# Kernel tuning notes

Measured on AMD Instinct MI355X. Metric: run time of the kernel, lower is better.

The kernel has to match this reference:

```python
import jax, jax.numpy as jnp
import numpy as np
from jax import lax

EPS = 1e-8
TAU = 1.0  # step=0 < tau_warmup_steps -> tau = tau_init


def setup_inputs() -> dict:
    key = jax.random.key(0)
    k1, k2 = jax.random.split(key)
    B, D, H, W = 4, 256, 32, 32
    C, K, d = 8, 1024, 32  # n_codebooks, vocab_size, codebook_dim (D = C*d)
    z = jax.random.normal(k1, (B, D, H, W), dtype=jnp.float32)
    cb = jax.random.normal(k2, (C, K, d), dtype=jnp.float32)
    cb = cb / (jnp.linalg.norm(cb, axis=-1, keepdims=True) + 1e-12) * np.sqrt(d).astype(np.float32)
    return {"z": z, "codebooks": cb}


def reference(z, codebooks):
    # Training-mode forward of LGQuantizer (step=0).
    B, D, H, W = z.shape
    C, K, d = codebooks.shape
    # (b d h w) -> (b h w) (c d_sub): chunk along channel dim
    zf = z.transpose(0, 2, 3, 1).reshape(-1, C, d)  # [N, C, d]
    N = zf.shape[0]

    # pairwise squared distances per codebook: [N, C, K]
    z_sq = jnp.sum(zf * zf, axis=-1)                      # [N, C]
    cb_sq = jnp.sum(codebooks * codebooks, axis=-1)       # [C, K]
    cross = jnp.einsum('ncd,ckd->nck', zf, codebooks)     # [N, C, K]
    dists = z_sq[:, :, None] - 2.0 * cross + cb_sq[None, :, :]

    inv_temp = 1.0 / (2.0 * TAU * TAU + EPS)
    logits = -dists * inv_temp
    q = jax.nn.softmax(logits, axis=-1)                   # [N, C, K]

    # soft quantization + straight-through with hard lookup
    z_q = jnp.einsum('nck,ckd->ncd', q, codebooks)        # [N, C, d]
    idx = jnp.argmin(dists, axis=-1)                      # [N, C]
    z_q_hard = codebooks[jnp.arange(C)[None, :], idx]     # [N, C, d]
    z_q_st = z_q + lax.stop_gradient(z_q_hard - z_q)

    quantized = z_q_st.reshape(B, H, W, D).transpose(0, 3, 1, 2)  # [B, D, H, W]
    indices = idx.reshape(B, H, W, C).transpose(0, 3, 1, 2)       # [B, C, H, W]

    # commitment: mse(z_part, q.detach() @ cb.detach()), averaged over codebooks
    commitment = jnp.mean((zf - lax.stop_gradient(z_q)) ** 2)

    log_q = jnp.log(q + EPS)
    neg_ent = jnp.sum(q * log_q, axis=-1)                 # [N, C]
    expected_dist = jnp.mean(jnp.sum(q * dists, axis=-1), axis=0)  # [C]
    kl_uniform = jnp.mean(neg_ent, axis=0) + np.log(K).astype(np.float32)  # [C]
    free_energy = jnp.mean(expected_dist * inv_temp + kl_uniform)

    confidence_loss = jnp.mean(-neg_ent)

    q_bar = jnp.mean(q, axis=0)                           # [C, K]
    balance_loss = jnp.mean(jnp.sum(q_bar * jnp.log(q_bar * K + EPS), axis=-1))

    return (quantized, indices, q, commitment, free_energy,
            confidence_loss, balance_loss, jnp.float32(TAU))
```

## Files before the change

kernel.cpp:

```cpp
#include <hip/hip_runtime.h>

#define WS_A0 0
#define WS_A1 1
#define WS_A2 2
#define WS_QBAR 16
#define WS_CBSQ (WS_QBAR + 8192)
#define WS_IDX  (WS_CBSQ + 8192)

#define OUT_IDX  1048576
#define OUT_Q    1081344
#define OUT_SCAL 34635776

__global__ __launch_bounds__(256) void k_cbsq(const float* __restrict__ cb,
                                              float* __restrict__ ws_f) {
  int i = blockIdx.x * 256 + threadIdx.x;
  const float* r = cb + (size_t)i * 32;
  float s = 0.f;
#pragma unroll
  for (int d = 0; d < 32; ++d) s = fmaf(r[d], r[d], s);
  ws_f[WS_CBSQ + i] = s;
}

__device__ __forceinline__ float wsum64(float v) {
#pragma unroll
  for (int m = 32; m >= 1; m >>= 1) v += __shfl_xor(v, m, 64);
  return v;
}

__device__ __forceinline__ float uread(float v) {
  return __int_as_float(__builtin_amdgcn_readfirstlane(__float_as_int(v)));
}

#define ZLD 33
__global__ __launch_bounds__(1024, 4)
void k_main(
    const float* __restrict__ z, const float* __restrict__ cb,
    float* __restrict__ out, float* __restrict__ ws_f, int* __restrict__ ws_i) {
  __shared__ __attribute__((aligned(16))) float smem[39040];
  float* cb_lds   = smem;
  float* qsum     = smem + 32768;
  float* cbsq_lds = smem + 33792;
  float* z_lds    = smem + 34816;

  const int c    = blockIdx.x >> 5;
  const int nblk = blockIdx.x & 31;
  const int tid  = threadIdx.x;
  const int lane = tid & 63;
  const int wave = tid >> 6;

  const int bb   = (nblk * 128) >> 10;
  const int hwb  = (nblk * 128) & 1023;

  const float4* cb4 = (const float4*)(cb + (size_t)c * 32768);
  float4* lds4 = (float4*)cb_lds;
#pragma unroll
  for (int i = 0; i < 8; ++i) {
    int idx = i * 1024 + tid;
    int k = idx >> 3, q = idx & 7;
    lds4[(k << 3) + (q ^ (k & 7))] = cb4[idx];
  }
  qsum[tid] = 0.f;
  cbsq_lds[tid] = ws_f[WS_CBSQ + c * 1024 + tid];
  {
    const float* zbase = z + (((size_t)bb * 256 + c * 32) << 10) + hwb;
#pragma unroll
    for (int i = 0; i < 4; ++i) {
      int idx = i * 1024 + tid;
      int d = idx >> 7, j = idx & 127;
      z_lds[j * ZLD + d] = zbase[(size_t)d * 1024 + j];
    }
  }
  __syncthreads();

  float* out_q   = out + OUT_Q;
  float* out_idx = out + OUT_IDX;

  float accA0 = 0.f, accA1 = 0.f, accA2 = 0.f;
  const int kl7 = lane & 7;

#pragma unroll 1
  for (int pp = 0; pp < 4; ++pp) {
    const int nl0 = wave * 8 + pp * 2;
    const int nl1 = nl0 + 1;
    const int n0 = nblk * 128 + nl0;
    const int n1 = n0 + 1;

    float zv0[32], zv1[32];
#pragma unroll
    for (int d = 0; d < 32; ++d) {
      zv0[d] = uread(z_lds[nl0 * ZLD + d]);
      zv1[d] = uread(z_lds[nl1 * ZLD + d]);
    }
    float zs0 = 0.f, zs1 = 0.f;
#pragma unroll
    for (int d = 0; d < 32; ++d) {
      zs0 = fmaf(zv0[d], zv0[d], zs0);
      zs1 = fmaf(zv1[d], zv1[d], zs1);
    }

    float e0[16], e1[16];
    float S0 = 0.f, S1 = 0.f, es0 = 0.f, es1 = 0.f;
    float sm0 = -INFINITY, sm1 = -INFINITY;
    int km0 = 0, km1 = 0;

#pragma unroll 2
    for (int jj = 0; jj < 16; ++jj) {
      const int k = jj * 64 + lane;
      float cq = cbsq_lds[k];
      float a0 = 0.f, a1 = 0.f;
      float g0 = 0.f, g1 = 0.f;
#pragma unroll
      for (int q = 0; q < 8; ++q) {
        float4 r4 = lds4[(k << 3) + (q ^ kl7)];
        a0 = fmaf(r4.x, zv0[q * 4 + 0], a0);
        a1 = fmaf(r4.y, zv0[q * 4 + 1], a1);
        a0 = fmaf(r4.z, zv0[q * 4 + 2], a0);
        a1 = fmaf(r4.w, zv0[q * 4 + 3], a1);
        g0 = fmaf(r4.x, zv1[q * 4 + 0], g0);
        g1 = fmaf(r4.y, zv1[q * 4 + 1], g1);
        g0 = fmaf(r4.z, zv1[q * 4 + 2], g0);
        g1 = fmaf(r4.w, zv1[q * 4 + 3], g1);
      }
      float s0 = (a0 + a1) - 0.5f * cq;
      float s1 = (g0 + g1) - 0.5f * cq;
      float ev0 = __expf(s0), ev1 = __expf(s1);
      e0[jj] = ev0; e1[jj] = ev1;
      S0 += ev0;  S1 += ev1;
      es0 = fmaf(ev0, s0, es0);
      es1 = fmaf(ev1, s1, es1);
      if (s0 > sm0) { sm0 = s0; km0 = k; }
      if (s1 > sm1) { sm1 = s1; km1 = k; }
    }

    float St0 = wsum64(S0), St1 = wsum64(S1);
    float rS0 = 1.f / St0, rS1 = 1.f / St1;
    float est0 = wsum64(es0), est1 = wsum64(es1);

    accA1 += (zs0 - 2.f * est0 * rS0) + (zs1 - 2.f * est1 * rS1);
    accA2 += (est0 * rS0 - __logf(St0)) + (est1 * rS1 - __logf(St1));

#pragma unroll
    for (int m = 32; m >= 1; m >>= 1) {
      float so = __shfl_xor(sm0, m, 64); int ko = __shfl_xor(km0, m, 64);
      if (so > sm0 || (so == sm0 && ko < km0)) { sm0 = so; km0 = ko; }
      float sp = __shfl_xor(sm1, m, 64); int kp = __shfl_xor(km1, m, 64);
      if (sp > sm1 || (sp == sm1 && kp < km1)) { sm1 = sp; km1 = kp; }
    }
    if (lane == 0) {
      out_idx[(size_t)bb * 8192 + c * 1024 + hwb + nl0] = (float)km0;
      ws_i[WS_IDX + n0 * 8 + c] = km0;
      out_idx[(size_t)bb * 8192 + c * 1024 + hwb + nl1] = (float)km1;
      ws_i[WS_IDX + n1 * 8 + c] = km1;
    }

    float* qp0 = out_q + ((size_t)n0 * 8 + c) * 1024;
    float* qp1 = out_q + ((size_t)n1 * 8 + c) * 1024;
#pragma unroll 2
    for (int jj = 0; jj < 16; ++jj) {
      float qv0 = e0[jj] * rS0;
      float qv1 = e1[jj] * rS1;
      qp0[jj * 64 + lane] = qv0;
      qp1[jj * 64 + lane] = qv1;
      atomicAdd(&qsum[jj * 64 + lane], qv0 + qv1);
    }

    float dA0, dA1;
    {
      float zqA0[16], zqA1[16];
#pragma unroll
      for (int i = 0; i < 16; ++i) { zqA0[i] = 0.f; zqA1[i] = 0.f; }
#pragma unroll 2
      for (int jj = 0; jj < 16; ++jj) {
        const int k = jj * 64 + lane;
        float qv0 = qp0[jj * 64 + lane];
        float qv1 = qp1[jj * 64 + lane];
#pragma unroll
        for (int q = 0; q < 4; ++q) {
          float4 r4 = lds4[(k << 3) + (q ^ kl7)];
          zqA0[q * 4 + 0] = fmaf(qv0, r4.x, zqA0[q * 4 + 0]);
          zqA0[q * 4 + 1] = fmaf(qv0, r4.y, zqA0[q * 4 + 1]);
          zqA0[q * 4 + 2] = fmaf(qv0, r4.z, zqA0[q * 4 + 2]);
          zqA0[q * 4 + 3] = fmaf(qv0, r4.w, zqA0[q * 4 + 3]);
          zqA1[q * 4 + 0] = fmaf(qv1, r4.x, zqA1[q * 4 + 0]);
          zqA1[q * 4 + 1] = fmaf(qv1, r4.y, zqA1[q * 4 + 1]);
          zqA1[q * 4 + 2] = fmaf(qv1, r4.z, zqA1[q * 4 + 2]);
          zqA1[q * 4 + 3] = fmaf(qv1, r4.w, zqA1[q * 4 + 3]);
        }
      }
#pragma unroll
      for (int t = 0; t < 4; ++t) {
        const int half = 8 >> t;
        const int up = (lane >> (5 - t)) & 1;
#pragma unroll
        for (int i = 0; i < half; ++i) {
          float sa0 = up ? zqA0[i] : zqA0[i + half];
          float ka0 = up ? zqA0[i + half] : zqA0[i];
          zqA0[i] = ka0 + __shfl_xor(sa0, 32 >> t, 64);
          float sa1 = up ? zqA1[i] : zqA1[i + half];
          float ka1 = up ? zqA1[i + half] : zqA1[i];
          zqA1[i] = ka1 + __shfl_xor(sa1, 32 >> t, 64);
        }
      }
      zqA0[0] += __shfl_xor(zqA0[0], 2, 64);
      zqA0[0] += __shfl_xor(zqA0[0], 1, 64);
      zqA1[0] += __shfl_xor(zqA1[0], 2, 64);
      zqA1[0] += __shfl_xor(zqA1[0], 1, 64);
      const int ddA = (lane >> 2) & 15;
      dA0 = z_lds[nl0 * ZLD + ddA] - zqA0[0];
      dA1 = z_lds[nl1 * ZLD + ddA] - zqA1[0];
    }

    float dB0, dB1;
    {
      float zqB0[16], zqB1[16];
#pragma unroll
      for (int i = 0; i < 16; ++i) { zqB0[i] = 0.f; zqB1[i] = 0.f; }
#pragma unroll 2
      for (int jj = 0; jj < 16; ++jj) {
        const int k = jj * 64 + lane;
        float qv0 = qp0[jj * 64 + lane];
        float qv1 = qp1[jj * 64 + lane];
#pragma unroll
        for (int q = 4; q < 8; ++q) {
          float4 r4 = lds4[(k << 3) + (q ^ kl7)];
          const int i0 = (q - 4) * 4;
          zqB0[i0 + 0] = fmaf(qv0, r4.x, zqB0[i0 + 0]);
          zqB0[i0 + 1] = fmaf(qv0, r4.y, zqB0[i0 + 1]);
          zqB0[i0 + 2] = fmaf(qv0, r4.z, zqB0[i0 + 2]);
          zqB0[i0 + 3] = fmaf(qv0, r4.w, zqB0[i0 + 3]);
          zqB1[i0 + 0] = fmaf(qv1, r4.x, zqB1[i0 + 0]);
          zqB1[i0 + 1] = fmaf(qv1, r4.y, zqB1[i0 + 1]);
          zqB1[i0 + 2] = fmaf(qv1, r4.z, zqB1[i0 + 2]);
          zqB1[i0 + 3] = fmaf(qv1, r4.w, zqB1[i0 + 3]);
        }
      }
#pragma unroll
      for (int t = 0; t < 4; ++t) {
        const int half = 8 >> t;
        const int up = (lane >> (5 - t)) & 1;
#pragma unroll
        for (int i = 0; i < half; ++i) {
          float sa0 = up ? zqB0[i] : zqB0[i + half];
          float ka0 = up ? zqB0[i + half] : zqB0[i];
          zqB0[i] = ka0 + __shfl_xor(sa0, 32 >> t, 64);
          float sa1 = up ? zqB1[i] : zqB1[i + half];
          float ka1 = up ? zqB1[i + half] : zqB1[i];
          zqB1[i] = ka1 + __shfl_xor(sa1, 32 >> t, 64);
        }
      }
      zqB0[0] += __shfl_xor(zqB0[0], 2, 64);
      zqB0[0] += __shfl_xor(zqB0[0], 1, 64);
      zqB1[0] += __shfl_xor(zqB1[0], 2, 64);
      zqB1[0] += __shfl_xor(zqB1[0], 1, 64);
      const int ddB = (lane >> 2) & 15;
      dB0 = z_lds[nl0 * ZLD + 16 + ddB] - zqB0[0];
      dB1 = z_lds[nl1 * ZLD + 16 + ddB] - zqB1[0];
    }

    accA0 += 0.25f * wsum64(dA0 * dA0 + dA1 * dA1 + dB0 * dB0 + dB1 * dB1);
  }

  if (lane == 0) {
    atomicAdd(&ws_f[WS_A0], accA0);
    atomicAdd(&ws_f[WS_A1], accA1);
    atomicAdd(&ws_f[WS_A2], accA2);
  }

  __syncthreads();
  atomicAdd(&ws_f[WS_QBAR + c * 1024 + tid], qsum[tid]);
}

__global__ __launch_bounds__(256) void k_hard(const float* __restrict__ cb,
                                              const int* __restrict__ ws_i,
                                              float* __restrict__ out0) {
  int o = blockIdx.x * 256 + threadIdx.x;
  int b  = o >> 18;
  int r  = o & 262143;
  int ch = r >> 10;
  int hw = r & 1023;
  int c = ch >> 5, dd = ch & 31;
  int n = (b << 10) + hw;
  int k = ws_i[WS_IDX + n * 8 + c];
  out0[o] = cb[((size_t)(c << 10) + k) * 32 + dd];
}

__global__ __launch_bounds__(256) void k_final(const float* __restrict__ ws_f,
                                               float* __restrict__ out_s) {
  __shared__ float red[256];
  int tid = threadIdx.x;
  float bal = 0.f;
  for (int i = tid; i < 8192; i += 256) {
    float qb = ws_f[WS_QBAR + i] * (1.0f / 4096.0f);
    bal += qb * __logf(qb * 1024.0f + 1e-8f);
  }
  red[tid] = bal;
  __syncthreads();
  for (int s = 128; s > 0; s >>= 1) {
    if (tid < s) red[tid] += red[tid + s];
    __syncthreads();
  }
  if (tid == 0) {
    float A0 = ws_f[WS_A0], A1 = ws_f[WS_A1], A2 = ws_f[WS_A2];
    out_s[0] = A0 * (1.0f / 1048576.0f);
    out_s[1] = (0.5f * A1 + A2) * (1.0f / 32768.0f) + 6.93147180559945f;
    out_s[2] = -A2 * (1.0f / 32768.0f);
    out_s[3] = red[0] * 0.125f;
    out_s[4] = 1.0f;
  }
}

extern "C" void kernel_launch(void* const* d_in, const int* in_sizes, int n_in,
                              void* d_out, int out_size, void* d_ws, size_t ws_size,
                              hipStream_t stream) {
  (void)in_sizes; (void)n_in; (void)out_size; (void)ws_size;
  const float* z  = (const float*)d_in[0];
  const float* cb = (const float*)d_in[1];
  float* out  = (float*)d_out;
  float* ws_f = (float*)d_ws;
  int*   ws_i = (int*)d_ws;

  hipMemsetAsync(d_ws, 0, (WS_QBAR + 8192) * sizeof(float), stream);
  k_cbsq <<<32,   256, 0, stream>>>(cb, ws_f);
  k_main <<<256, 1024, 0, stream>>>(z, cb, out, ws_f, ws_i);
  k_hard <<<4096, 256, 0, stream>>>(cb, ws_i, out);
  k_final<<<1,    256, 0, stream>>>(ws_f, out + OUT_SCAL);
}
```

Measured before the change: 504.7 us.

## Fuse soft-quantization accumulation into distance passes, recompute logits instead of storing exps

The per-row loop becomes two passes over the codebook. The first pass computes the logits and exp sums and also accumulates the first half of the unnormalized z_q, scaled by 1/S afterwards. The second pass recomputes the logits, writes normalized q with nontemporal stores, tracks the argmax, and accumulates the second half of z_q. This drops the 16-entry exp register arrays and the re-read of q from global memory, at the cost of computing the distance dot products twice. Register pressure should fall and occupancy may rise, but extra FMAs and LDS reads are added.

```diff
diff --git a/kernel.cpp b/kernel.cpp
--- a/kernel.cpp
+++ b/kernel.cpp
@@ -98,20 +98,19 @@
       zs1 = fmaf(zv1[d], zv1[d], zs1);
     }
 
-    float e0[16], e1[16];
     float S0 = 0.f, S1 = 0.f, es0 = 0.f, es1 = 0.f;
-    float sm0 = -INFINITY, sm1 = -INFINITY;
-    int km0 = 0, km1 = 0;
-
-#pragma unroll 2
+    float zqA0[16], zqA1[16];
+#pragma unroll
+    for (int i = 0; i < 16; ++i) { zqA0[i] = 0.f; zqA1[i] = 0.f; }
+
+#pragma unroll 1
     for (int jj = 0; jj < 16; ++jj) {
       const int k = jj * 64 + lane;
-      float cq = cbsq_lds[k];
-      float a0 = 0.f, a1 = 0.f;
-      float g0 = 0.f, g1 = 0.f;
+      const int kbase = k << 3;
+      float a0 = 0.f, a1 = 0.f, g0 = 0.f, g1 = 0.f;
 #pragma unroll
       for (int q = 0; q < 8; ++q) {
-        float4 r4 = lds4[(k << 3) + (q ^ kl7)];
+        float4 r4 = lds4[kbase + (q ^ kl7)];
         a0 = fmaf(r4.x, zv0[q * 4 + 0], a0);
         a1 = fmaf(r4.y, zv0[q * 4 + 1], a1);
         a0 = fmaf(r4.z, zv0[q * 4 + 2], a0);
@@ -121,15 +120,25 @@
         g0 = fmaf(r4.z, zv1[q * 4 + 2], g0);
         g1 = fmaf(r4.w, zv1[q * 4 + 3], g1);
       }
+      float cq = cbsq_lds[k];
       float s0 = (a0 + a1) - 0.5f * cq;
       float s1 = (g0 + g1) - 0.5f * cq;
       float ev0 = __expf(s0), ev1 = __expf(s1);
-      e0[jj] = ev0; e1[jj] = ev1;
       S0 += ev0;  S1 += ev1;
       es0 = fmaf(ev0, s0, es0);
       es1 = fmaf(ev1, s1, es1);
-      if (s0 > sm0) { sm0 = s0; km0 = k; }
-      if (s1 > sm1) { sm1 = s1; km1 = k; }
+#pragma unroll
+      for (int q = 0; q < 4; ++q) {
+        float4 r4 = lds4[kbase + (q ^ kl7)];
+        zqA0[q * 4 + 0] = fmaf(ev0, r4.x, zqA0[q * 4 + 0]);
+        zqA0[q * 4 + 1] = fmaf(ev0, r4.y, zqA0[q * 4 + 1]);
+        zqA0[q * 4 + 2] = fmaf(ev0, r4.z, zqA0[q * 4 + 2]);
+        zqA0[q * 4 + 3] = fmaf(ev0, r4.w, zqA0[q * 4 + 3]);
+        zqA1[q * 4 + 0] = fmaf(ev1, r4.x, zqA1[q * 4 + 0]);
+        zqA1[q * 4 + 1] = fmaf(ev1, r4.y, zqA1[q * 4 + 1]);
+        zqA1[q * 4 + 2] = fmaf(ev1, r4.z, zqA1[q * 4 + 2]);
+        zqA1[q * 4 + 3] = fmaf(ev1, r4.w, zqA1[q * 4 + 3]);
+      }
     }
 
     float St0 = wsum64(S0), St1 = wsum64(S1);
@@ -139,54 +148,7 @@
     accA1 += (zs0 - 2.f * est0 * rS0) + (zs1 - 2.f * est1 * rS1);
     accA2 += (est0 * rS0 - __logf(St0)) + (est1 * rS1 - __logf(St1));
 
-#pragma unroll
-    for (int m = 32; m >= 1; m >>= 1) {
-      float so = __shfl_xor(sm0, m, 64); int ko = __shfl_xor(km0, m, 64);
-      if (so > sm0 || (so == sm0 && ko < km0)) { sm0 = so; km0 = ko; }
-      float sp = __shfl_xor(sm1, m, 64); int kp = __shfl_xor(km1, m, 64);
-      if (sp > sm1 || (sp == sm1 && kp < km1)) { sm1 = sp; km1 = kp; }
-    }
-    if (lane == 0) {
-      out_idx[(size_t)bb * 8192 + c * 1024 + hwb + nl0] = (float)km0;
-      ws_i[WS_IDX + n0 * 8 + c] = km0;
-      out_idx[(size_t)bb * 8192 + c * 1024 + hwb + nl1] = (float)km1;
-      ws_i[WS_IDX + n1 * 8 + c] = km1;
-    }
-
-    float* qp0 = out_q + ((size_t)n0 * 8 + c) * 1024;
-    float* qp1 = out_q + ((size_t)n1 * 8 + c) * 1024;
-#pragma unroll 2
-    for (int jj = 0; jj < 16; ++jj) {
-      float qv0 = e0[jj] * rS0;
-      float qv1 = e1[jj] * rS1;
-      qp0[jj * 64 + lane] = qv0;
-      qp1[jj * 64 + lane] = qv1;
-      atomicAdd(&qsum[jj * 64 + lane], qv0 + qv1);
-    }
-
-    float dA0, dA1;
     {
-      float zqA0[16], zqA1[16];
-#pragma unroll
-      for (int i = 0; i < 16; ++i) { zqA0[i] = 0.f; zqA1[i] = 0.f; }
-#pragma unroll 2
-      for (int jj = 0; jj < 16; ++jj) {
-        const int k = jj * 64 + lane;
-        float qv0 = qp0[jj * 64 + lane];
-        float qv1 = qp1[jj * 64 + lane];
-#pragma unroll
-        for (int q = 0; q < 4; ++q) {
-          float4 r4 = lds4[(k << 3) + (q ^ kl7)];
-          zqA0[q * 4 + 0] = fmaf(qv0, r4.x, zqA0[q * 4 + 0]);
-          zqA0[q * 4 + 1] = fmaf(qv0, r4.y, zqA0[q * 4 + 1]);
-          zqA0[q * 4 + 2] = fmaf(qv0, r4.z, zqA0[q * 4 + 2]);
-          zqA0[q * 4 + 3] = fmaf(qv0, r4.w, zqA0[q * 4 + 3]);
-          zqA1[q * 4 + 0] = fmaf(qv1, r4.x, zqA1[q * 4 + 0]);
-          zqA1[q * 4 + 1] = fmaf(qv1, r4.y, zqA1[q * 4 + 1]);
-          zqA1[q * 4 + 2] = fmaf(qv1, r4.z, zqA1[q * 4 + 2]);
-          zqA1[q * 4 + 3] = fmaf(qv1, r4.w, zqA1[q * 4 + 3]);
-        }
-      }
 #pragma unroll
       for (int t = 0; t < 4; ++t) {
         const int half = 8 >> t;
@@ -206,58 +168,97 @@
       zqA1[0] += __shfl_xor(zqA1[0], 2, 64);
       zqA1[0] += __shfl_xor(zqA1[0], 1, 64);
       const int ddA = (lane >> 2) & 15;
-      dA0 = z_lds[nl0 * ZLD + ddA] - zqA0[0];
-      dA1 = z_lds[nl1 * ZLD + ddA] - zqA1[0];
-    }
-
-    float dB0, dB1;
-    {
-      float zqB0[16], zqB1[16];
-#pragma unroll
-      for (int i = 0; i < 16; ++i) { zqB0[i] = 0.f; zqB1[i] = 0.f; }
-#pragma unroll 2
-      for (int jj = 0; jj < 16; ++jj) {
-        const int k = jj * 64 + lane;
-        float qv0 = qp0[jj * 64 + lane];
-        float qv1 = qp1[jj * 64 + lane];
-#pragma unroll
-        for (int q = 4; q < 8; ++q) {
-          float4 r4 = lds4[(k << 3) + (q ^ kl7)];
-          const int i0 = (q - 4) * 4;
-          zqB0[i0 + 0] = fmaf(qv0, r4.x, zqB0[i0 + 0]);
-          zqB0[i0 + 1] = fmaf(qv0, r4.y, zqB0[i0 + 1]);
-          zqB0[i0 + 2] = fmaf(qv0, r4.z, zqB0[i0 + 2]);
-          zqB0[i0 + 3] = fmaf(qv0, r4.w, zqB0[i0 + 3]);
-          zqB1[i0 + 0] = fmaf(qv1, r4.x, zqB1[i0 + 0]);
-          zqB1[i0 + 1] = fmaf(qv1, r4.y, zqB1[i0 + 1]);
-          zqB1[i0 + 2] = fmaf(qv1, r4.z, zqB1[i0 + 2]);
-          zqB1[i0 + 3] = fmaf(qv1, r4.w, zqB1[i0 + 3]);
-        }
-      }
-#pragma unroll
-      for (int t = 0; t < 4; ++t) {
-        const int half = 8 >> t;
-        const int up = (lane >> (5 - t)) & 1;
-#pragma unroll
-        for (int i = 0; i < half; ++i) {
-          float sa0 = up ? zqB0[i] : zqB0[i + half];
-          float ka0 = up ? zqB0[i + half] : zqB0[i];
-          zqB0[i] = ka0 + __shfl_xor(sa0, 32 >> t, 64);
-          float sa1 = up ? zqB1[i] : zqB1[i + half];
-          float ka1 = up ? zqB1[i + half] : zqB1[i];
-          zqB1[i] = ka1 + __shfl_xor(sa1, 32 >> t, 64);
-        }
-      }
-      zqB0[0] += __shfl_xor(zqB0[0], 2, 64);
-      zqB0[0] += __shfl_xor(zqB0[0], 1, 64);
-      zqB1[0] += __shfl_xor(zqB1[0], 2, 64);
-      zqB1[0] += __shfl_xor(zqB1[0], 1, 64);
-      const int ddB = (lane >> 2) & 15;
-      dB0 = z_lds[nl0 * ZLD + 16 + ddB] - zqB0[0];
-      dB1 = z_lds[nl1 * ZLD + 16 + ddB] - zqB1[0];
-    }
-
-    accA0 += 0.25f * wsum64(dA0 * dA0 + dA1 * dA1 + dB0 * dB0 + dB1 * dB1);
+      float dA0 = z_lds[nl0 * ZLD + ddA] - zqA0[0] * rS0;
+      float dA1 = z_lds[nl1 * ZLD + ddA] - zqA1[0] * rS1;
+      accA0 += 0.25f * wsum64(dA0 * dA0 + dA1 * dA1);
+    }
+
+    float sm0 = -INFINITY, sm1 = -INFINITY;
+    int km0 = 0, km1 = 0;
+    float zqB0[16], zqB1[16];
+#pragma unroll
+    for (int i = 0; i < 16; ++i) { zqB0[i] = 0.f; zqB1[i] = 0.f; }
+    float* qp0 = out_q + ((size_t)n0 * 8 + c) * 1024;
+    float* qp1 = out_q + ((size_t)n1 * 8 + c) * 1024;
+
+#pragma unroll 1
+    for (int jj = 0; jj < 16; ++jj) {
+      const int k = jj * 64 + lane;
+      const int kbase = k << 3;
+      float a0 = 0.f, a1 = 0.f, g0 = 0.f, g1 = 0.f;
+#pragma unroll
+      for (int q = 0; q < 8; ++q) {
+        float4 r4 = lds4[kbase + (q ^ kl7)];
+        a0 = fmaf(r4.x, zv0[q * 4 + 0], a0);
+        a1 = fmaf(r4.y, zv0[q * 4 + 1], a1);
+        a0 = fmaf(r4.z, zv0[q * 4 + 2], a0);
+        a1 = fmaf(r4.w, zv0[q * 4 + 3], a1);
+        g0 = fmaf(r4.x, zv1[q * 4 + 0], g0);
+        g1 = fmaf(r4.y, zv1[q * 4 + 1], g1);
+        g0 = fmaf(r4.z, zv1[q * 4 + 2], g0);
+        g1 = fmaf(r4.w, zv1[q * 4 + 3], g1);
+      }
+      float cq = cbsq_lds[k];
+      float s0 = (a0 + a1) - 0.5f * cq;
+      float s1 = (g0 + g1) - 0.5f * cq;
+      if (s0 > sm0) { sm0 = s0; km0 = k; }
+      if (s1 > sm1) { sm1 = s1; km1 = k; }
+      float qv0 = __expf(s0) * rS0;
+      float qv1 = __expf(s1) * rS1;
+      __builtin_nontemporal_store(qv0, qp0 + jj * 64 + lane);
+      __builtin_nontemporal_store(qv1, qp1 + jj * 64 + lane);
+      atomicAdd(&qsum[jj * 64 + lane], qv0 + qv1);
+#pragma unroll
+      for (int q = 4; q < 8; ++q) {
+        float4 r4 = lds4[kbase + (q ^ kl7)];
+        const int i0 = (q - 4) * 4;
+        zqB0[i0 + 0] = fmaf(qv0, r4.x, zqB0[i0 + 0]);
+        zqB0[i0 + 1] = fmaf(qv0, r4.y, zqB0[i0 + 1]);
+        zqB0[i0 + 2] = fmaf(qv0, r4.z, zqB0[i0 + 2]);
+        zqB0[i0 + 3] = fmaf(qv0, r4.w, zqB0[i0 + 3]);
+        zqB1[i0 + 0] = fmaf(qv1, r4.x, zqB1[i0 + 0]);
+        zqB1[i0 + 1] = fmaf(qv1, r4.y, zqB1[i0 + 1]);
+        zqB1[i0 + 2] = fmaf(qv1, r4.z, zqB1[i0 + 2]);
+        zqB1[i0 + 3] = fmaf(qv1, r4.w, zqB1[i0 + 3]);
+      }
+    }
+
+#pragma unroll
+    for (int m = 32; m >= 1; m >>= 1) {
+      float so = __shfl_xor(sm0, m, 64); int ko = __shfl_xor(km0, m, 64);
+      if (so > sm0 || (so == sm0 && ko < km0)) { sm0 = so; km0 = ko; }
+      float sp = __shfl_xor(sm1, m, 64); int kp = __shfl_xor(km1, m, 64);
+      if (sp > sm1 || (sp == sm1 && kp < km1)) { sm1 = sp; km1 = kp; }
+    }
+    if (lane == 0) {
+      out_idx[(size_t)bb * 8192 + c * 1024 + hwb + nl0] = (float)km0;
+      ws_i[WS_IDX + n0 * 8 + c] = km0;
+      out_idx[(size_t)bb * 8192 + c * 1024 + hwb + nl1] = (float)km1;
+      ws_i[WS_IDX + n1 * 8 + c] = km1;
+    }
+
+#pragma unroll
+    for (int t = 0; t < 4; ++t) {
+      const int half = 8 >> t;
+      const int up = (lane >> (5 - t)) & 1;
+#pragma unroll
+      for (int i = 0; i < half; ++i) {
+        float sa0 = up ? zqB0[i] : zqB0[i + half];
+        float ka0 = up ? zqB0[i + half] : zqB0[i];
+        zqB0[i] = ka0 + __shfl_xor(sa0, 32 >> t, 64);
+        float sa1 = up ? zqB1[i] : zqB1[i + half];
+        float ka1 = up ? zqB1[i + half] : zqB1[i];
+        zqB1[i] = ka1 + __shfl_xor(sa1, 32 >> t, 64);
+      }
+    }
+    zqB0[0] += __shfl_xor(zqB0[0], 2, 64);
+    zqB0[0] += __shfl_xor(zqB0[0], 1, 64);
+    zqB1[0] += __shfl_xor(zqB1[0], 2, 64);
+    zqB1[0] += __shfl_xor(zqB1[0], 1, 64);
+    const int ddB = (lane >> 2) & 15;
+    float dB0 = z_lds[nl0 * ZLD + 16 + ddB] - zqB0[0];
+    float dB1 = z_lds[nl1 * ZLD + 16 + ddB] - zqB1[0];
+    accA0 += 0.25f * wsum64(dB0 * dB0 + dB1 * dB1);
   }
 
   if (lane == 0) {
```

After: 481.7 us. -4.5%, faster.
